# Optimization experiments

Measured on AMD Instinct MI355X. Metric: run time of the kernel, lower is better.

## Reference

```python
import jax, jax.numpy as jnp
import numpy as np

N, E, NFEAT, NHID, NCLASS = 50000, 800000, 8, 128, 112
SMOOTH = 0.5          # smoo init arg
NEG_SLOPE_ATT = 0.2   # LeakyReLU slope inside sparse attention (SpGAT convention)
NEG_SLOPE_OUT = 0.01  # F.leaky_relu default in the outer loop
EPS = 1e-16


def setup_inputs() -> dict:
    key = jax.random.key(0)
    ks = jax.random.split(key, 12)
    g = lambda k, shape, s=0.1: jax.random.normal(k, shape, dtype=jnp.float32) * s
    return {
        "x": jax.random.normal(ks[0], (N, NFEAT), dtype=jnp.float32),
        "edge_index": jax.random.randint(ks[1], (2, E), 0, N, dtype=jnp.int64) if jax.config.jax_enable_x64 else jax.random.randint(ks[1], (2, E), 0, N, dtype=jnp.int32),
        "edge_weight": jax.random.uniform(ks[2], (E,), dtype=jnp.float32),
        # ScattterAttentionLayer 1: nfeat -> nhid (weight W, attention vector a split into src/dst halves)
        "W1": g(ks[3], (NFEAT, NHID)),
        "a1_src": g(ks[4], (NHID,)),
        "a1_dst": g(ks[5], (NHID,)),
        # ScattterAttentionLayer 2: nhid -> nhid
        "W2": g(ks[6], (NHID, NHID)),
        "a2_src": g(ks[7], (NHID,)),
        "a2_dst": g(ks[8], (NHID,)),
        # shared BatchNorm1d(nhid)
        "gamma": jnp.ones((NHID,), jnp.float32),
        "beta": jnp.zeros((NHID,), jnp.float32),
        # GC_withres: nhid -> nclass
        "Wg": g(ks[9], (NHID, NCLASS)),
        "bg": jnp.zeros((NCLASS,), jnp.float32),
    }


def scatter_attention(h_in, W, a_src, a_dst, src, dst):
    """Sparse GAT-style scatter attention (SpGraphAttentionLayer math).
    score_ij = exp(-leakyrelu(a_src.h_i + a_dst.h_j)); softmax-normalized per dst node."""
    h = h_in @ W                                   # [N, F]
    f_src = h @ a_src                              # [N]
    f_dst = h @ a_dst                              # [N]
    e = jnp.exp(-jax.nn.leaky_relu(f_src[src] + f_dst[dst], NEG_SLOPE_ATT))  # [E]
    denom = jax.ops.segment_sum(e, dst, num_segments=N) + EPS                # [N]
    num = jax.ops.segment_sum(e[:, None] * h[src], dst, num_segments=N)      # [N, F]
    return num / denom[:, None]


def batchnorm(x, gamma, beta):
    mu = x.mean(axis=0)
    var = x.var(axis=0)
    return (x - mu) * jax.lax.rsqrt(var + 1e-5) * gamma + beta


def reference(x, edge_index, edge_weight, W1, a1_src, a1_dst, W2, a2_src, a2_dst, gamma, beta, Wg, bg):
    src, dst = edge_index[0], edge_index[1]
    # conv loop (nlayers=3 -> two ScattterAttentionLayer convs), shared bn1, leaky_relu; dropout=identity (eval)
    h = scatter_attention(x, W1, a1_src, a1_dst, src, dst)
    h = jax.nn.leaky_relu(batchnorm(h, gamma, beta), NEG_SLOPE_OUT)
    h = scatter_attention(h, W2, a2_src, a2_dst, src, dst)
    h = jax.nn.leaky_relu(batchnorm(h, gamma, beta), NEG_SLOPE_OUT)
    # GC_withres: spmm((smooth*A + I)/(1+smooth), h @ Wg) + bias
    support = h @ Wg                               # [N, nclass]
    w = (SMOOTH / (1.0 + SMOOTH)) * edge_weight    # [E]
    agg = jax.ops.segment_sum(w[:, None] * support[src], dst, num_segments=N)
    return agg + support / (1.0 + SMOOTH) + bg
```

## Files before the change

kernel.cpp:

```cpp
#include <hip/hip_runtime.h>
#include <hip/hip_bf16.h>

#define N_NODES 50000
#define N_EDGES 800000
#define NFEAT   8
#define NHID    128
#define NCLASS  112
#define SEG_EPS 1e-16f
#define BN_EPS  1e-5f
#define CAP     64
#define MACRO_TILES 782
#define NODE_RANGE 6250
#define FILL_CHUNK 2048
#define FILL_CHUNKS 391
#define FSFD_BLOCKS 196
#define SG_GRID 3200
#define SG_IT 4
#define ATT_GRID 3200
#define ATT_IT 4
#define OUT_GRID 3200
#define OUT_IT 4

#define FILLB (FILL_CHUNKS * 8)
#define FSFD0 FILLB
#define W2P0  (FSFD0 + FSFD_BLOCKS)
#define W2T0  (W2P0 + 64)
#define WGT0  (W2T0 + 32)
#define GRID_FILL (WGT0 + 28)

typedef __hip_bfloat16 bf16;
typedef __attribute__((ext_vector_type(8))) short short8;
typedef __attribute__((ext_vector_type(4))) float f32x4;
typedef __attribute__((ext_vector_type(4))) unsigned int u32x4;

__device__ __forceinline__ float bfbits2f(unsigned int lo16) {
    union { unsigned int u; float f; } c; c.u = lo16 << 16; return c.f;
}

__device__ __forceinline__ unsigned int pack_bf2(float a, float b) {
    union { unsigned int u; bf16 h[2]; } t;
    t.h[0] = __float2bfloat16(a);
    t.h[1] = __float2bfloat16(b);
    return t.u;
}

__global__ __launch_bounds__(256)
void k_fill_fsfd(const int* __restrict__ src, const int* __restrict__ dst,
                 const float* __restrict__ ewt,
                 int* __restrict__ cnt, unsigned int* __restrict__ bucket,
                 const float* __restrict__ x, const float* __restrict__ W1,
                 const float* __restrict__ a1s, const float* __restrict__ a1d,
                 float* __restrict__ xf,
                 const float* __restrict__ W2,
                 const float* __restrict__ a2s, const float* __restrict__ a2d,
                 float* __restrict__ w2s, float* __restrict__ w2d,
                 const float* __restrict__ Wg,
                 bf16* __restrict__ W2t, bf16* __restrict__ Wgt) {
    __shared__ float sw[16];
    __shared__ float ps[4], pd[4];
    const int t = threadIdx.x;
    if (blockIdx.x < FILLB) {
        const int range = blockIdx.x & 7;
        const int chunk = blockIdx.x >> 3;
        const int lo = range * NODE_RANGE, hi = lo + NODE_RANGE;
        const int e0 = chunk * FILL_CHUNK + t * 8;
        if (e0 >= N_EDGES) return;
        const int4 d0 = *(const int4*)&dst[e0];
        const int4 d1 = *(const int4*)&dst[e0 + 4];
        const int dd[8] = {d0.x, d0.y, d0.z, d0.w, d1.x, d1.y, d1.z, d1.w};
#pragma unroll
        for (int i = 0; i < 8; i++) {
            int d = dd[i];
            if (d < lo || d >= hi) continue;
            int e = e0 + i;
            int slot = atomicAdd(&cnt[d], 1);
            if (slot < CAP) {
                unsigned int iw = (unsigned int)(ewt[e] * 32767.f + 0.5f);
                bucket[d * CAP + slot] = ((unsigned int)src[e] << 15) | iw;
            }
        }
        return;
    }
    if (blockIdx.x < W2P0) {
        const int w = t >> 6, lane = t & 63;
#pragma unroll
        for (int dd = 0; dd < 4; dd++) {
            int dot = w + dd * 4;
            int k = dot & 7;
            const float* a = (dot < 8) ? a1s : a1d;
            float v = W1[k * NHID + lane] * a[lane] + W1[k * NHID + 64 + lane] * a[64 + lane];
#pragma unroll
            for (int off = 32; off > 0; off >>= 1) v += __shfl_down(v, off);
            if (lane == 0) sw[dot] = v;
        }
        __syncthreads();
        const int i = (blockIdx.x - FSFD0) * 256 + t;
        if (i < N_NODES) {
            const float4 x0 = ((const float4*)x)[i * 2];
            const float4 x1 = ((const float4*)x)[i * 2 + 1];
            float fsv = x0.x*sw[0] + x0.y*sw[1] + x0.z*sw[2] + x0.w*sw[3]
                      + x1.x*sw[4] + x1.y*sw[5] + x1.z*sw[6] + x1.w*sw[7];
            float fdv = x0.x*sw[8] + x0.y*sw[9] + x0.z*sw[10] + x0.w*sw[11]
                      + x1.x*sw[12] + x1.y*sw[13] + x1.z*sw[14] + x1.w*sw[15];
            float4* xr = (float4*)&xf[(size_t)i * 16];
            xr[0] = x0;
            xr[1] = x1;
            xr[2] = make_float4(fsv, fdv, 0.f, 0.f);
        }
        return;
    }
    if (blockIdx.x < W2T0) {
        const int k = (blockIdx.x - W2P0) * 2 + (t >> 7);
        const int n = t & 127;
        float wv = W2[k * NHID + n];
        float vs = wv * a2s[n], vd = wv * a2d[n];
#pragma unroll
        for (int off = 32; off > 0; off >>= 1) { vs += __shfl_down(vs, off); vd += __shfl_down(vd, off); }
        const int wid = t >> 6;
        if ((t & 63) == 0) { ps[wid] = vs; pd[wid] = vd; }
        __syncthreads();
        if ((t & 127) == 0) { w2s[k] = ps[wid] + ps[wid + 1]; w2d[k] = pd[wid] + pd[wid + 1]; }
        return;
    }
    if (blockIdx.x < WGT0) {
        const int n = (blockIdx.x - W2T0) * 4 + (t >> 6);
        const int k2 = (t & 63) * 2;
        *(unsigned int*)&W2t[n * 128 + k2] = pack_bf2(W2[k2 * NHID + n], W2[(k2 + 1) * NHID + n]);
        return;
    }
    const int n = (blockIdx.x - WGT0) * 4 + (t >> 6);
    const int k2 = (t & 63) * 2;
    *(unsigned int*)&Wgt[n * 128 + k2] = pack_bf2(Wg[k2 * NCLASS + n], Wg[(k2 + 1) * NCLASS + n]);
}

__global__ __launch_bounds__(256)
void k_sort_gather_y1(const int* __restrict__ cnt, unsigned int* __restrict__ bucket,
                      const float* __restrict__ xf, const float* __restrict__ W1,
                      bf16* __restrict__ y1,
                      float* __restrict__ Psum, float* __restrict__ Psq) {
    const int xcd = blockIdx.x & 7;
    const int wb  = blockIdx.x >> 3;
    const int t = threadIdx.x;
    const int q = t >> 6;
    const int lane = t & 63;
    float w1c0[8], w1c1[8];
#pragma unroll
    for (int k = 0; k < 8; k++) {
        const float2 wv = *(const float2*)&W1[k * NHID + 2 * lane];
        w1c0[k] = wv.x; w1c1[k] = wv.y;
    }
    float ls0 = 0.f, ls1 = 0.f, lq0 = 0.f, lq1 = 0.f;
    for (int it = 0; it < SG_IT; it++) {
        const int ni = (wb + it * 400) * 4 + q;
        if (ni >= NODE_RANGE) continue;
        const int d = xcd * NODE_RANGE + ni;
        const int deg = min(cnt[d], CAP);
        unsigned int v = (lane < deg) ? bucket[d * CAP + lane] : 0xFFFFFFFFu;
#pragma unroll
        for (int k = 2; k <= 64; k <<= 1) {
#pragma unroll
            for (int s = k >> 1; s > 0; s >>= 1) {
                unsigned int o = (unsigned int)__shfl_xor((int)v, s);
                bool keepmin = ((lane & s) == 0) == ((lane & k) == 0);
                v = keepmin ? min(v, o) : max(v, o);
            }
        }
        if (lane < deg) bucket[d * CAP + lane] = v;
        const int epair = lane >> 1;
        const int half  = lane & 1;
        const float fdd = xf[(size_t)d * 16 + 9];
        float4 acc = {0.f, 0.f, 0.f, 0.f};
        float den = 0.f;
        for (int base = 0; base < deg; base += 32) {
            int e = base + epair;
            unsigned int u = (unsigned int)__shfl((int)v, e);
            if (e < deg) {
                int s = u >> 15;
                const float4 xv = *(const float4*)&xf[(size_t)s * 16 + half * 4];
                float fsv = xf[(size_t)s * 16 + 8];
                float f = fsv + fdd;
                float lr = f > 0.f ? f : 0.2f * f;
                float c = __expf(-lr);
                if (half == 0) den += c;
                acc.x += c * xv.x; acc.y += c * xv.y; acc.z += c * xv.z; acc.w += c * xv.w;
            }
        }
#pragma unroll
        for (int off = 2; off < 64; off <<= 1) {
            acc.x += __shfl_xor(acc.x, off);
            acc.y += __shfl_xor(acc.y, off);
            acc.z += __shfl_xor(acc.z, off);
            acc.w += __shfl_xor(acc.w, off);
            den   += __shfl_xor(den, off);
        }
        den += __shfl_xor(den, 1);
        float4 oth;
        oth.x = __shfl_xor(acc.x, 1);
        oth.y = __shfl_xor(acc.y, 1);
        oth.z = __shfl_xor(acc.z, 1);
        oth.w = __shfl_xor(acc.w, 1);
        const float r = 1.f / (den + SEG_EPS);
        float xa[8];
        if ((lane & 1) == 0) {
            xa[0]=acc.x*r; xa[1]=acc.y*r; xa[2]=acc.z*r; xa[3]=acc.w*r;
            xa[4]=oth.x*r; xa[5]=oth.y*r; xa[6]=oth.z*r; xa[7]=oth.w*r;
        } else {
            xa[0]=oth.x*r; xa[1]=oth.y*r; xa[2]=oth.z*r; xa[3]=oth.w*r;
            xa[4]=acc.x*r; xa[5]=acc.y*r; xa[6]=acc.z*r; xa[7]=acc.w*r;
        }
        float v0 = 0.f, v1 = 0.f;
#pragma unroll
        for (int k = 0; k < 8; k++) {
            v0 += xa[k] * w1c0[k];
            v1 += xa[k] * w1c1[k];
        }
        ((unsigned int*)y1)[(size_t)d * 64 + lane] = pack_bf2(v0, v1);
        ls0 += v0; lq0 += v0 * v0;
        ls1 += v1; lq1 += v1 * v1;
    }
    __shared__ float sred[4][64][2];
    sred[q][lane][0] = ls0;
    sred[q][lane][1] = ls1;
    __syncthreads();
    if (t < 128) {
        int ln = t >> 1, cp = t & 1;
        Psum[blockIdx.x * 128 + t] =
            ((sred[0][ln][cp] + sred[1][ln][cp]) + sred[2][ln][cp]) + sred[3][ln][cp];
    }
    __syncthreads();
    sred[q][lane][0] = lq0;
    sred[q][lane][1] = lq1;
    __syncthreads();
    if (t < 128) {
        int ln = t >> 1, cp = t & 1;
        Psq[blockIdx.x * 128 + t] =
            ((sred[0][ln][cp] + sred[1][ln][cp]) + sred[2][ln][cp]) + sred[3][ln][cp];
    }
}

__global__ __launch_bounds__(256)
void k_reduce_fused(const float* __restrict__ Psum, const float* __restrict__ Psq,
                    int nIn, int chunk,
                    float* __restrict__ Qsum, float* __restrict__ Qsq,
                    const float* __restrict__ gamma, const float* __restrict__ beta,
                    float* __restrict__ scale, float* __restrict__ shift,
                    int* __restrict__ flag) {
    const int t = threadIdx.x;
    if (blockIdx.x < 16) {
        const int j = t & 127;
        const int h = t >> 7;
        const int u = blockIdx.x * 2 + h;
        const int b0 = u * chunk, b1 = min(b0 + chunk, nIn);
        float s = 0.f, q = 0.f;
#pragma unroll 8
        for (int b = b0; b < b1; b++) {
            s += Psum[b * 128 + j];
            q += Psq[b * 128 + j];
        }
        Qsum[u * 128 + j] = s;
        Qsq[u * 128 + j] = q;
        __threadfence();
        __syncthreads();
        if (t == 0) atomicAdd(flag, 1);
        return;
    }
    if (t == 0) { while (atomicAdd(flag, 0) < 16) { } }
    __syncthreads();
    __threadfence();
    const int j = t & 127;
    const int g = t >> 7;
    float s = 0.f, q = 0.f;
#pragma unroll
    for (int u = g * 16; u < g * 16 + 16; u++) {
        s += Qsum[u * 128 + j];
        q += Qsq[u * 128 + j];
    }
    __shared__ float Ls[2][128], Lq[2][128];
    Ls[g][j] = s; Lq[g][j] = q;
    __syncthreads();
    if (g == 0) {
        float st = Ls[0][j] + Ls[1][j];
        float qt = Lq[0][j] + Lq[1][j];
        float mu = st * (1.f / N_NODES);
        float var = qt * (1.f / N_NODES) - mu * mu;
        float rs = rsqrtf(var + BN_EPS);
        float ga = gamma[j];
        scale[j] = rs * ga;
        shift[j] = beta[j] - mu * rs * ga;
    }
    __syncthreads();
    if (t == 0) atomicExch(flag, 0);
}

template<int NCV, bool ATT>
__global__ __launch_bounds__(256)
void k_gemm_mfma(const bf16* __restrict__ Yin,
                 const float* __restrict__ scale, const float* __restrict__ shift,
                 const bf16* __restrict__ Wt_g,
                 bf16* __restrict__ hout,
                 const float* __restrict__ w2s, const float* __restrict__ w2d,
                 float* __restrict__ fs, float* __restrict__ fd) {
    constexpr int NT = NCV / 16;
    __shared__ bf16 Wt[NCV * 136];
    __shared__ float scb[128], shb[128];
    const int t = threadIdx.x;
    for (int idx = t; idx < NCV * 16; idx += 256) {
        int n = idx >> 4, c = idx & 15;
        *(u32x4*)&Wt[n * 136 + c * 8] = *(const u32x4*)&Wt_g[n * 128 + c * 8];
    }
    if (t < 128) { scb[t] = scale[t]; shb[t] = shift[t]; }
    const int lane = t & 63;
    const int m16 = lane & 15;
    const int g = lane >> 4;
    const int rg = t >> 6;
    short8 attb[4];
    if constexpr (ATT) {
#pragma unroll
        for (int kk = 0; kk < 4; kk++) {
            union { short8 s; unsigned int u[4]; } pk;
            if (m16 < 2) {
                const float* wv = (m16 == 0) ? w2s : w2d;
                const float4 f0 = *(const float4*)&wv[kk * 32 + g * 8];
                const float4 f1 = *(const float4*)&wv[kk * 32 + g * 8 + 4];
                pk.u[0] = pack_bf2(f0.x, f0.y);
                pk.u[1] = pack_bf2(f0.z, f0.w);
                pk.u[2] = pack_bf2(f1.x, f1.y);
                pk.u[3] = pack_bf2(f1.z, f1.w);
            } else {
                pk.u[0] = pk.u[1] = pk.u[2] = pk.u[3] = 0u;
            }
            attb[kk] = pk.s;
        }
    }
    __syncthreads();

    const int row0 = blockIdx.x * 64;
    const int arow = row0 + rg * 16 + m16;
    const bool rok = arow < N_NODES;
    f32x4 acc[NT];
#pragma unroll
    for (int c = 0; c < NT; c++) acc[c] = (f32x4){0.f, 0.f, 0.f, 0.f};
    f32x4 accA = (f32x4){0.f, 0.f, 0.f, 0.f};
#pragma unroll
    for (int kk = 0; kk < 4; kk++) {
        u32x4 u4 = rok
            ? *(const u32x4*)&((const unsigned int*)Yin)[(size_t)arow * 64 + kk * 16 + g * 4]
            : (u32x4){0u, 0u, 0u, 0u};
        const float4 s0 = *(const float4*)&scb[kk * 32 + g * 8];
        const float4 s1 = *(const float4*)&scb[kk * 32 + g * 8 + 4];
        const float4 h0 = *(const float4*)&shb[kk * 32 + g * 8];
        const float4 h1 = *(const float4*)&shb[kk * 32 + g * 8 + 4];
        const float scv[8] = {s0.x, s0.y, s0.z, s0.w, s1.x, s1.y, s1.z, s1.w};
        const float shv[8] = {h0.x, h0.y, h0.z, h0.w, h1.x, h1.y, h1.z, h1.w};
        union { short8 s; unsigned int u[4]; } A;
#pragma unroll
        for (int fq = 0; fq < 4; fq++) {
            unsigned int u = u4[fq];
            float v0 = bfbits2f(u & 0xFFFF) * scv[2*fq]   + shv[2*fq];   v0 = v0 > 0.f ? v0 : 0.01f * v0;
            float v1 = bfbits2f(u >> 16)    * scv[2*fq+1] + shv[2*fq+1]; v1 = v1 > 0.f ? v1 : 0.01f * v1;
            A.u[fq] = pack_bf2(v0, v1);
        }
#pragma unroll
        for (int c = 0; c < NT; c++) {
            short8 bfr = *(const short8*)&Wt[(c * 16 + m16) * 136 + kk * 32 + g * 8];
            acc[c] = __builtin_amdgcn_mfma_f32_16x16x32_bf16(A.s, bfr, acc[c], 0, 0, 0);
        }
        if constexpr (ATT)
            accA = __builtin_amdgcn_mfma_f32_16x16x32_bf16(A.s, attb[kk], accA, 0, 0, 0);
    }
    const int orow = row0 + rg * 16 + g * 4;
#pragma unroll
    for (int c = 0; c < NT; c++) {
#pragma unroll
        for (int r = 0; r < 4; r++) {
            int grow = orow + r;
            if (grow < N_NODES)
                hout[(size_t)grow * 128 + c * 16 + m16] = __float2bfloat16(acc[c][r]);
        }
    }
    if constexpr (ATT) {
        if (m16 < 2) {
            float* o = (m16 == 0) ? fs : fd;
#pragma unroll
            for (int r = 0; r < 4; r++) {
                int grow = orow + r;
                if (grow < N_NODES) o[grow] = accA[r];
            }
        }
    }
}

__global__ __launch_bounds__(256)
void k_gather_attn_bf(const int* __restrict__ cnt, const unsigned int* __restrict__ bucket,
                      const float* __restrict__ fs, const float* __restrict__ fd,
                      const bf16* __restrict__ h, bf16* __restrict__ y,
                      float* __restrict__ Psum, float* __restrict__ Psq) {
    const int xcd = blockIdx.x & 7;
    const int wb  = blockIdx.x >> 3;
    const int t = threadIdx.x;
    const int q = t >> 6;
    const int lane = t & 63;
    const int grp = lane >> 4;
    const int l = lane & 15;
    __shared__ int s_idx[4][CAP];
    __shared__ float s_e[4][CAP];
    __shared__ float sred[4][16][8];
    float ls[8], lq[8];
#pragma unroll
    for (int i = 0; i < 8; i++) { ls[i] = 0.f; lq[i] = 0.f; }

    for (int it = 0; it < ATT_IT; it++) {
        const int ni = (wb + it * 400) * 4 + q;
        if (ni >= NODE_RANGE) continue;
        const int d = xcd * NODE_RANGE + ni;
        const int deg = min(cnt[d], CAP);
        const float fdd = fd[d];
        if (lane < deg) {
            int s = bucket[d * CAP + lane] >> 15;
            float f = fs[s] + fdd;
            float lr = f > 0.f ? f : 0.2f * f;
            s_idx[q][lane] = s;
            s_e[q][lane] = __expf(-lr);
        }
        float a[8];
#pragma unroll
        for (int i = 0; i < 8; i++) a[i] = 0.f;
        float den = 0.f;
#pragma unroll 4
        for (int base = 0; base < deg; base += 4) {
            int k = base + grp;
            bool ev = k < deg;
            int kk = ev ? k : 0;
            float e = ev ? s_e[q][kk] : 0.f;
            int sidx = s_idx[q][kk];
            u32x4 u4 = *(const u32x4*)&((const unsigned int*)h)[(size_t)sidx * 64 + l * 4];
            den += e;
#pragma unroll
            for (int fq = 0; fq < 4; fq++) {
                unsigned int u = u4[fq];
                a[2*fq]   += e * bfbits2f(u & 0xFFFF);
                a[2*fq+1] += e * bfbits2f(u >> 16);
            }
        }
#pragma unroll
        for (int off = 16; off < 64; off <<= 1) {
#pragma unroll
            for (int i = 0; i < 8; i++) a[i] += __shfl_xor(a[i], off);
            den += __shfl_xor(den, off);
        }
        float r = 1.f / (den + SEG_EPS);
        if (lane < 16) {
            u32x4 pk;
#pragma unroll
            for (int fq = 0; fq < 4; fq++) {
                float v0 = a[2*fq] * r, v1 = a[2*fq+1] * r;
                pk[fq] = pack_bf2(v0, v1);
                ls[2*fq] += v0;   lq[2*fq] += v0 * v0;
                ls[2*fq+1] += v1; lq[2*fq+1] += v1 * v1;
            }
            *(u32x4*)&((unsigned int*)y)[(size_t)d * 64 + l * 4] = pk;
        }
    }
    if (lane < 16) {
#pragma unroll
        for (int i = 0; i < 8; i++) sred[q][l][i] = ls[i];
    }
    __syncthreads();
    if (t < 128) {
        int l16 = t >> 3, i8 = t & 7;
        Psum[blockIdx.x * 128 + t] =
            ((sred[0][l16][i8] + sred[1][l16][i8]) + sred[2][l16][i8]) + sred[3][l16][i8];
    }
    __syncthreads();
    if (lane < 16) {
#pragma unroll
        for (int i = 0; i < 8; i++) sred[q][l][i] = lq[i];
    }
    __syncthreads();
    if (t < 128) {
        int l16 = t >> 3, i8 = t & 7;
        Psq[blockIdx.x * 128 + t] =
            ((sred[0][l16][i8] + sred[1][l16][i8]) + sred[2][l16][i8]) + sred[3][l16][i8];
    }
}

__global__ __launch_bounds__(256)
void k_gather_out_bf(const int* __restrict__ cnt, const unsigned int* __restrict__ bucket,
                     const bf16* __restrict__ sup, const float* __restrict__ bg,
                     float* __restrict__ out) {
    const int xcd = blockIdx.x & 7;
    const int wb  = blockIdx.x >> 3;
    const int t = threadIdx.x;
    const int q = t >> 6;
    const int lane = t & 63;
    const int grp = lane >> 4;
    const int l = lane & 15;
    __shared__ int s_idx[4][CAP];
    __shared__ float s_w[4][CAP];
    for (int it = 0; it < OUT_IT; it++) {
        const int ni = (wb + it * 400) * 4 + q;
        if (ni >= NODE_RANGE) continue;
        const int d = xcd * NODE_RANGE + ni;
        const int deg = min(cnt[d], CAP);
        if (lane < deg) {
            unsigned int b = bucket[d * CAP + lane];
            s_idx[q][lane] = b >> 15;
            s_w[q][lane] = (float)(b & 0x7FFF) * (1.f / (32767.f * 3.f));
        }
        float a[8];
#pragma unroll
        for (int i = 0; i < 8; i++) a[i] = 0.f;
#pragma unroll 4
        for (int base = 0; base < deg; base += 4) {
            int k = base + grp;
            bool ev = k < deg;
            int kk = ev ? k : 0;
            float w = ev ? s_w[q][kk] : 0.f;
            int sidx = s_idx[q][kk];
            u32x4 u4 = (l < 14)
                ? *(const u32x4*)&((const unsigned int*)sup)[(size_t)sidx * 64 + l * 4]
                : (u32x4){0u, 0u, 0u, 0u};
#pragma unroll
            for (int fq = 0; fq < 4; fq++) {
                unsigned int u = u4[fq];
                a[2*fq]   += w * bfbits2f(u & 0xFFFF);
                a[2*fq+1] += w * bfbits2f(u >> 16);
            }
        }
#pragma unroll
        for (int off = 16; off < 64; off <<= 1) {
#pragma unroll
            for (int i = 0; i < 8; i++) a[i] += __shfl_xor(a[i], off);
        }
        if (l < 14) {
            u32x4 us = *(const u32x4*)&((const unsigned int*)sup)[(size_t)d * 64 + l * 4];
            const float4 b0 = *(const float4*)&bg[l * 8];
            const float4 b1 = *(const float4*)&bg[l * 8 + 4];
            float4 o0, o1;
            o0.x = a[0] + bfbits2f(us[0] & 0xFFFF) * (2.f/3.f) + b0.x;
            o0.y = a[1] + bfbits2f(us[0] >> 16)    * (2.f/3.f) + b0.y;
            o0.z = a[2] + bfbits2f(us[1] & 0xFFFF) * (2.f/3.f) + b0.z;
            o0.w = a[3] + bfbits2f(us[1] >> 16)    * (2.f/3.f) + b0.w;
            o1.x = a[4] + bfbits2f(us[2] & 0xFFFF) * (2.f/3.f) + b1.x;
            o1.y = a[5] + bfbits2f(us[2] >> 16)    * (2.f/3.f) + b1.y;
            o1.z = a[6] + bfbits2f(us[3] & 0xFFFF) * (2.f/3.f) + b1.z;
            o1.w = a[7] + bfbits2f(us[3] >> 16)    * (2.f/3.f) + b1.w;
            *(float4*)&out[(size_t)d * NCLASS + l * 8]     = o0;
            *(float4*)&out[(size_t)d * NCLASS + l * 8 + 4] = o1;
        }
    }
}

extern "C" void kernel_launch(void* const* d_in, const int* in_sizes, int n_in,
                              void* d_out, int out_size, void* d_ws, size_t ws_size,
                              hipStream_t stream) {
    const float* x    = (const float*)d_in[0];
    const int*   ei   = (const int*)d_in[1];
    const float* ewt  = (const float*)d_in[2];
    const float* W1   = (const float*)d_in[3];
    const float* a1s  = (const float*)d_in[4];
    const float* a1d  = (const float*)d_in[5];
    const float* W2   = (const float*)d_in[6];
    const float* a2s  = (const float*)d_in[7];
    const float* a2d  = (const float*)d_in[8];
    const float* gam  = (const float*)d_in[9];
    const float* bet  = (const float*)d_in[10];
    const float* Wg   = (const float*)d_in[11];
    const float* bg   = (const float*)d_in[12];
    float* out = (float*)d_out;

    const int* src = ei;
    const int* dst = ei + N_EDGES;

    float* ws    = (float*)d_ws;
    bf16*  Yb    = (bf16*)ws;
    bf16*  Hb    = (bf16*)(ws + 3203072);
    unsigned int* bucket = (unsigned int*)(ws + 6403072);
    float* fs    = ws + 10003072;
    float* fd    = ws + 10053072;
    int*   cnt   = (int*)(ws + 10103072);
    int*   flags = (int*)(ws + 10153072);
    float* scale = ws + 10153076;
    float* shift = scale + 128;
    float* w2s   = shift + 128;
    float* w2d   = w2s + 128;
    float* Psum  = ws + 10153600;
    float* Psq   = Psum + 409600;
    float* Qsum  = Psq + 409600;
    float* Qsq   = Qsum + 4096;
    bf16*  W2t   = (bf16*)(Qsq + 4096);
    bf16*  Wgt   = W2t + 16384;
    float* xf    = ws + 10996352;

    hipMemsetAsync(cnt, 0, (size_t)(N_NODES + 4) * 4, stream);
    k_fill_fsfd<<<GRID_FILL, 256, 0, stream>>>(
        src, dst, ewt, cnt, bucket, x, W1, a1s, a1d, xf,
        W2, a2s, a2d, w2s, w2d, Wg, W2t, Wgt);

    k_sort_gather_y1<<<SG_GRID, 256, 0, stream>>>(cnt, bucket, xf, W1,
                                                  Yb, Psum, Psq);
    k_reduce_fused<<<17, 256, 0, stream>>>(Psum, Psq, SG_GRID, 100, Qsum, Qsq,
                                           gam, bet, scale, shift, flags + 0);

    k_gemm_mfma<128, true><<<MACRO_TILES, 256, 0, stream>>>(Yb, scale, shift, W2t, Hb,
                                                            w2s, w2d, fs, fd);
    k_gather_attn_bf<<<ATT_GRID, 256, 0, stream>>>(cnt, bucket, fs, fd, Hb, Yb,
                                                   Psum, Psq);
    k_reduce_fused<<<17, 256, 0, stream>>>(Psum, Psq, ATT_GRID, 100, Qsum, Qsq,
                                           gam, bet, scale, shift, flags + 1);

    k_gemm_mfma<112, false><<<MACRO_TILES, 256, 0, stream>>>(Yb, scale, shift, Wgt, Hb,
                                                             nullptr, nullptr, nullptr, nullptr);
    k_gather_out_bf<<<OUT_GRID, 256, 0, stream>>>(cnt, bucket, Hb, bg, out);
}
```

Measured before the change: 277.1 us.

## Fuse BatchNorm stat reduction into gather kernels via tail blocks and counters

Removes the two separate k_reduce_fused launches by appending 17 tail blocks to the y1 gather and attention gather kernels. Producer blocks bump an atomic counter after writing their partial sums, and the tail blocks spin-wait with s_sleep until all producers finish before doing the two-level reduction. The flag region is enlarged and now zeroed by the existing memset, so the old reset-to-zero step is dropped. Separately, the fill kernel loads src and edge weights with vector loads and packs them before the atomic scatter. The spin-wait depends on the tail blocks being scheduled after, or alongside, the producers; if they occupy CU slots early, they hold resources while waiting.

Measured after the change: 828.9 us. 2.99x slower.

```diff
diff --git a/kernel.cpp b/kernel.cpp
--- a/kernel.cpp
+++ b/kernel.cpp
@@ -20,6 +20,7 @@
 #define ATT_IT 4
 #define OUT_GRID 3200
 #define OUT_IT 4
+#define RED_CHUNK 100
 
 #define FILLB (FILL_CHUNKS * 8)
 #define FSFD0 FILLB
@@ -42,6 +43,59 @@
     t.h[0] = __float2bfloat16(a);
     t.h[1] = __float2bfloat16(b);
     return t.u;
+}
+
+__device__ __forceinline__ void bn_reduce_tail(
+        int tailIdx, int t, int nProd,
+        const float* __restrict__ Psum, const float* __restrict__ Psq,
+        float* __restrict__ Qsum, float* __restrict__ Qsq,
+        const float* __restrict__ gamma, const float* __restrict__ beta,
+        float* __restrict__ scale, float* __restrict__ shift,
+        int* __restrict__ fl) {
+    if (tailIdx < 16) {
+        if (t == 0) { while (atomicAdd(&fl[0], 0) < nProd) __builtin_amdgcn_s_sleep(8); }
+        __syncthreads();
+        __threadfence();
+        const int j = t & 127;
+        const int u = tailIdx * 2 + (t >> 7);
+        const int b0 = u * RED_CHUNK, b1 = b0 + RED_CHUNK;
+        float s = 0.f, q = 0.f;
+#pragma unroll 8
+        for (int b = b0; b < b1; b++) {
+            s += Psum[b * 128 + j];
+            q += Psq[b * 128 + j];
+        }
+        Qsum[u * 128 + j] = s;
+        Qsq[u * 128 + j] = q;
+        __threadfence();
+        __syncthreads();
+        if (t == 0) atomicAdd(&fl[16], 1);
+        return;
+    }
+    if (t == 0) { while (atomicAdd(&fl[16], 0) < 16) __builtin_amdgcn_s_sleep(8); }
+    __syncthreads();
+    __threadfence();
+    const int j = t & 127;
+    const int g = t >> 7;
+    float s = 0.f, q = 0.f;
+#pragma unroll
+    for (int u = g * 16; u < g * 16 + 16; u++) {
+        s += Qsum[u * 128 + j];
+        q += Qsq[u * 128 + j];
+    }
+    __shared__ float Ls[2][128], Lq[2][128];
+    Ls[g][j] = s; Lq[g][j] = q;
+    __syncthreads();
+    if (g == 0) {
+        float st = Ls[0][j] + Ls[1][j];
+        float qt = Lq[0][j] + Lq[1][j];
+        float mu = st * (1.f / N_NODES);
+        float var = qt * (1.f / N_NODES) - mu * mu;
+        float rs = rsqrtf(var + BN_EPS);
+        float ga = gamma[j];
+        scale[j] = rs * ga;
+        shift[j] = beta[j] - mu * rs * ga;
+    }
 }
 
 __global__ __launch_bounds__(256)
@@ -67,17 +121,24 @@
         if (e0 >= N_EDGES) return;
         const int4 d0 = *(const int4*)&dst[e0];
         const int4 d1 = *(const int4*)&dst[e0 + 4];
+        const int4 s0 = *(const int4*)&src[e0];
+        const int4 s1 = *(const int4*)&src[e0 + 4];
+        const float4 w0 = *(const float4*)&ewt[e0];
+        const float4 w1 = *(const float4*)&ewt[e0 + 4];
         const int dd[8] = {d0.x, d0.y, d0.z, d0.w, d1.x, d1.y, d1.z, d1.w};
+        const int ss[8] = {s0.x, s0.y, s0.z, s0.w, s1.x, s1.y, s1.z, s1.w};
+        const float ww[8] = {w0.x, w0.y, w0.z, w0.w, w1.x, w1.y, w1.z, w1.w};
+        unsigned int pl[8];
+#pragma unroll
+        for (int i = 0; i < 8; i++)
+            pl[i] = ((unsigned int)ss[i] << 15) |
+                    (unsigned int)(ww[i] * 32767.f + 0.5f);
 #pragma unroll
         for (int i = 0; i < 8; i++) {
             int d = dd[i];
             if (d < lo || d >= hi) continue;
-            int e = e0 + i;
             int slot = atomicAdd(&cnt[d], 1);
-            if (slot < CAP) {
-                unsigned int iw = (unsigned int)(ewt[e] * 32767.f + 0.5f);
-                bucket[d * CAP + slot] = ((unsigned int)src[e] << 15) | iw;
-            }
+            if (slot < CAP) bucket[d * CAP + slot] = pl[i];
         }
         return;
     }
@@ -137,10 +198,19 @@
 void k_sort_gather_y1(const int* __restrict__ cnt, unsigned int* __restrict__ bucket,
                       const float* __restrict__ xf, const float* __restrict__ W1,
                       bf16* __restrict__ y1,
-                      float* __restrict__ Psum, float* __restrict__ Psq) {
+                      float* __restrict__ Psum, float* __restrict__ Psq,
+                      float* __restrict__ Qsum, float* __restrict__ Qsq,
+                      const float* __restrict__ gamma, const float* __restrict__ beta,
+                      float* __restrict__ scale, float* __restrict__ shift,
+                      int* __restrict__ fl) {
+    const int t = threadIdx.x;
+    if (blockIdx.x >= SG_GRID) {
+        bn_reduce_tail(blockIdx.x - SG_GRID, t, SG_GRID,
+                       Psum, Psq, Qsum, Qsq, gamma, beta, scale, shift, fl);
+        return;
+    }
     const int xcd = blockIdx.x & 7;
     const int wb  = blockIdx.x >> 3;
-    const int t = threadIdx.x;
     const int q = t >> 6;
     const int lane = t & 63;
     float w1c0[8], w1c1[8];
@@ -236,60 +306,9 @@
         Psq[blockIdx.x * 128 + t] =
             ((sred[0][ln][cp] + sred[1][ln][cp]) + sred[2][ln][cp]) + sred[3][ln][cp];
     }
-}
-
-__global__ __launch_bounds__(256)
-void k_reduce_fused(const float* __restrict__ Psum, const float* __restrict__ Psq,
-                    int nIn, int chunk,
-                    float* __restrict__ Qsum, float* __restrict__ Qsq,
-                    const float* __restrict__ gamma, const float* __restrict__ beta,
-                    float* __restrict__ scale, float* __restrict__ shift,
-                    int* __restrict__ flag) {
-    const int t = threadIdx.x;
-    if (blockIdx.x < 16) {
-        const int j = t & 127;
-        const int h = t >> 7;
-        const int u = blockIdx.x * 2 + h;
-        const int b0 = u * chunk, b1 = min(b0 + chunk, nIn);
-        float s = 0.f, q = 0.f;
-#pragma unroll 8
-        for (int b = b0; b < b1; b++) {
-            s += Psum[b * 128 + j];
-            q += Psq[b * 128 + j];
-        }
-        Qsum[u * 128 + j] = s;
-        Qsq[u * 128 + j] = q;
-        __threadfence();
-        __syncthreads();
-        if (t == 0) atomicAdd(flag, 1);
-        return;
-    }
-    if (t == 0) { while (atomicAdd(flag, 0) < 16) { } }
-    __syncthreads();
     __threadfence();
-    const int j = t & 127;
-    const int g = t >> 7;
-    float s = 0.f, q = 0.f;
-#pragma unroll
-    for (int u = g * 16; u < g * 16 + 16; u++) {
-        s += Qsum[u * 128 + j];
-        q += Qsq[u * 128 + j];
-    }
-    __shared__ float Ls[2][128], Lq[2][128];
-    Ls[g][j] = s; Lq[g][j] = q;
-    __syncthreads();
-    if (g == 0) {
-        float st = Ls[0][j] + Ls[1][j];
-        float qt = Lq[0][j] + Lq[1][j];
-        float mu = st * (1.f / N_NODES);
-        float var = qt * (1.f / N_NODES) - mu * mu;
-        float rs = rsqrtf(var + BN_EPS);
-        float ga = gamma[j];
-        scale[j] = rs * ga;
-        shift[j] = beta[j] - mu * rs * ga;
-    }
-    __syncthreads();
-    if (t == 0) atomicExch(flag, 0);
+    __syncthreads();
+    if (t == 0) atomicAdd(&fl[0], 1);
 }
 
 template<int NCV, bool ATT>
@@ -394,10 +413,19 @@
 void k_gather_attn_bf(const int* __restrict__ cnt, const unsigned int* __restrict__ bucket,
                       const float* __restrict__ fs, const float* __restrict__ fd,
                       const bf16* __restrict__ h, bf16* __restrict__ y,
-                      float* __restrict__ Psum, float* __restrict__ Psq) {
+                      float* __restrict__ Psum, float* __restrict__ Psq,
+                      float* __restrict__ Qsum, float* __restrict__ Qsq,
+                      const float* __restrict__ gamma, const float* __restrict__ beta,
+                      float* __restrict__ scale, float* __restrict__ shift,
+                      int* __restrict__ fl) {
+    const int t = threadIdx.x;
+    if (blockIdx.x >= ATT_GRID) {
+        bn_reduce_tail(blockIdx.x - ATT_GRID, t, ATT_GRID,
+                       Psum, Psq, Qsum, Qsq, gamma, beta, scale, shift, fl);
+        return;
+    }
     const int xcd = blockIdx.x & 7;
     const int wb  = blockIdx.x >> 3;
-    const int t = threadIdx.x;
     const int q = t >> 6;
     const int lane = t & 63;
     const int grp = lane >> 4;
@@ -482,6 +510,9 @@
         Psq[blockIdx.x * 128 + t] =
             ((sred[0][l16][i8] + sred[1][l16][i8]) + sred[2][l16][i8]) + sred[3][l16][i8];
     }
+    __threadfence();
+    __syncthreads();
+    if (t == 0) atomicAdd(&fl[0], 1);
 }
 
 __global__ __launch_bounds__(256)
@@ -579,35 +610,33 @@
     float* fs    = ws + 10003072;
     float* fd    = ws + 10053072;
     int*   cnt   = (int*)(ws + 10103072);
-    int*   flags = (int*)(ws + 10153072);
-    float* scale = ws + 10153076;
+    int*   fl    = (int*)(ws + 10153072);
+    float* scale = ws + 10153584;
     float* shift = scale + 128;
     float* w2s   = shift + 128;
     float* w2d   = w2s + 128;
-    float* Psum  = ws + 10153600;
+    float* Psum  = ws + 10154112;
     float* Psq   = Psum + 409600;
     float* Qsum  = Psq + 409600;
     float* Qsq   = Qsum + 4096;
     bf16*  W2t   = (bf16*)(Qsq + 4096);
     bf16*  Wgt   = W2t + 16384;
-    float* xf    = ws + 10996352;
-
-    hipMemsetAsync(cnt, 0, (size_t)(N_NODES + 4) * 4, stream);
+    float* xf    = ws + 11000000;
+
+    hipMemsetAsync(cnt, 0, (size_t)(N_NODES + 512) * 4, stream);
     k_fill_fsfd<<<GRID_FILL, 256, 0, stream>>>(
         src, dst, ewt, cnt, bucket, x, W1, a1s, a1d, xf,
         W2, a2s, a2d, w2s, w2d, Wg, W2t, Wgt);
 
-    k_sort_gather_y1<<<SG_GRID, 256, 0, stream>>>(cnt, bucket, xf, W1,
-                                                  Yb, Psum, Psq);
-    k_reduce_fused<<<17, 256, 0, stream>>>(Psum, Psq, SG_GRID, 100, Qsum, Qsq,
-                                           gam, bet, scale, shift, flags + 0);
+    k_sort_gather_y1<<<SG_GRID + 17, 256, 0, stream>>>(cnt, bucket, xf, W1,
+                                                       Yb, Psum, Psq, Qsum, Qsq,
+                                                       gam, bet, scale, shift, fl);
 
     k_gemm_mfma<128, true><<<MACRO_TILES, 256, 0, stream>>>(Yb, scale, shift, W2t, Hb,
                                                             w2s, w2d, fs, fd);
-    k_gather_attn_bf<<<ATT_GRID, 256, 0, stream>>>(cnt, bucket, fs, fd, Hb, Yb,
-                                                   Psum, Psq);
-    k_reduce_fused<<<17, 256, 0, stream>>>(Psum, Psq, ATT_GRID, 100, Qsum, Qsq,
-                                           gam, bet, scale, shift, flags + 1);
+    k_gather_attn_bf<<<ATT_GRID + 17, 256, 0, stream>>>(cnt, bucket, fs, fd, Hb, Yb,
+                                                        Psum, Psq, Qsum, Qsq,
+                                                        gam, bet, scale, shift, fl + 64);
 
     k_gemm_mfma<112, false><<<MACRO_TILES, 256, 0, stream>>>(Yb, scale, shift, Wgt, Hb,
                                                              nullptr, nullptr, nullptr, nullptr);
```
